# Kernel optimization log

Measured on AMD Instinct MI355X. Metric: run time of the kernel, lower is better.

## Reference

```python
import jax, jax.numpy as jnp
import numpy as np

N, F, H, G = 4096, 256, 8, 128  # atoms, filters, heads, groups
D = F // H  # head dim = 32


def setup_inputs() -> dict:
    key = jax.random.key(0)
    ks = jax.random.split(key, 12)
    x = jax.random.normal(ks[0], (N, F), dtype=jnp.float32)
    # sorted group ids in [0, G): block_diag over unique-count blocks == equality mask on sorted ids
    seg = jnp.sort(jax.random.randint(ks[1], (N,), 0, G, dtype=jnp.int32))
    elem_index = jnp.stack([jnp.arange(N, dtype=jnp.int32), seg])  # [2, N]
    s = 1.0 / np.sqrt(F)
    def lin(k):
        kw, kb = jax.random.split(k)
        return (jax.random.normal(kw, (F, F), dtype=jnp.float32) * s,
                jnp.zeros((F,), dtype=jnp.float32))
    Wq, bq = lin(ks[2]); Wk, bk = lin(ks[3]); Wv, bv = lin(ks[4])
    Wo1, bo1 = lin(ks[5]); Wo2, bo2 = lin(ks[6])
    return {"x": x, "elem_index": elem_index,
            "Wq": Wq, "bq": bq, "Wk": Wk, "bk": bk, "Wv": Wv, "bv": bv,
            "Wo1": Wo1, "bo1": bo1, "Wo2": Wo2, "bo2": bo2}


def reference(x, elem_index, Wq, bq, Wk, bk, Wv, bv, Wo1, bo1, Wo2, bo2):
    n = x.shape[0]
    # projections -> [H, N, D]
    q = (x @ Wq.T + bq).reshape(n, H, D).transpose(1, 0, 2)
    k = (x @ Wk.T + bk).reshape(n, H, D).transpose(1, 0, 2)
    v = (x @ Wv.T + bv).reshape(n, H, D).transpose(1, 0, 2)
    attn = jnp.einsum('hnd,hmd->hnm', q, k)          # [H, N, N]
    attn = jax.nn.silu(attn)                          # attn_act = activation() in source
    seg = elem_index[1]
    mask = (seg[:, None] == seg[None, :]).astype(attn.dtype)  # block-diagonal (sorted ids)
    attn = attn * mask
    out = jnp.einsum('hnm,hmd->hnd', attn, v)        # [H, N, D]
    out = out.transpose(1, 0, 2).reshape(n, F)       # [N, F]
    out = out @ Wo1.T + bo1
    out = jax.ops.segment_sum(out, seg, num_segments=G)  # scatter sum by group -> [G, F]
    out = out @ Wo2.T + bo2
    return jax.nn.silu(out)
```

## Files before the change

kernel.cpp:

```cpp
#include <hip/hip_runtime.h>
#include <math.h>

#define NATOMS 4096
#define FDIM   256
#define NHEAD  8
#define DHEAD  32
#define NGRP   128

typedef __bf16 bf16x8 __attribute__((ext_vector_type(8)));
typedef float  floatx4 __attribute__((ext_vector_type(4)));
typedef unsigned short u16x4 __attribute__((ext_vector_type(4)));

__device__ __forceinline__ float silu_f(float x) {
    return x / (1.0f + __expf(-x));
}

__device__ __forceinline__ unsigned short f2bf(float f) {
    union { float f; unsigned int u; } a;
    a.f = f;
    unsigned int r = a.u + 0x7FFF + ((a.u >> 16) & 1);
    return (unsigned short)(r >> 16);
}

__global__ __launch_bounds__(256) void prep_kernel(
    const float* __restrict__ x,
    const float* __restrict__ Wq, const float* __restrict__ Wk, const float* __restrict__ Wv,
    const float* __restrict__ bq, const float* __restrict__ bk, const float* __restrict__ bv,
    const int* __restrict__ seg,
    unsigned short* __restrict__ xb, unsigned short* __restrict__ Wb,
    float* __restrict__ b_all, int* __restrict__ off, float* __restrict__ cntf)
{
    int tid = threadIdx.x;
    unsigned int u = blockIdx.x * 256 + tid;

    if (blockIdx.x == 0 && tid < NGRP) {
        int g = tid;
        auto lb = [&](int val) {
            int lo = 0, hi = NATOMS;
            while (lo < hi) {
                int mid = (lo + hi) >> 1;
                if (seg[mid] < val) lo = mid + 1; else hi = mid;
            }
            return lo;
        };
        int a = lb(g);
        int b = lb(g + 1);
        off[g] = a;
        if (g == NGRP - 1) off[NGRP] = NATOMS;
        cntf[g] = (float)(b - a);
    }
    if (blockIdx.x == 1 && tid < 192) {
        const float* src = (tid < 64) ? bq : (tid < 128) ? bk : bv;
        int t = tid & 63;
        ((float4*)b_all)[tid] = ((const float4*)src)[t];
    }

    const unsigned int NX4 = 262144;
    const unsigned int NW4 = 16384;
    float4 fv;
    u16x4* dst;
    if (u < NX4) {
        fv = ((const float4*)x)[u];
        dst = (u16x4*)xb + u;
    } else {
        unsigned int r = u - NX4;
        unsigned int w = r / NW4;
        unsigned int i = r - w * NW4;
        const float* W = (w == 0) ? Wq : (w == 1) ? Wk : Wv;
        fv = ((const float4*)W)[i];
        dst = (u16x4*)Wb + (size_t)w * NW4 + i;
    }
    u16x4 o;
    o[0] = f2bf(fv.x); o[1] = f2bf(fv.y); o[2] = f2bf(fv.z); o[3] = f2bf(fv.w);
    *dst = o;
}

__global__ __launch_bounds__(256) void qkv_mfma(
    const unsigned short* __restrict__ xb, const unsigned short* __restrict__ Wb,
    const float* __restrict__ b_all, float* __restrict__ qkv)
{
    int tid = threadIdx.x;
    int lane = tid & 63;
    int ww = tid >> 6;
    int wrow = ww >> 1, wcol = ww & 1;
    int m_base = blockIdx.x * 64 + wrow * 32;
    int n_base = blockIdx.y * 128 + wcol * 64;

    int l15 = lane & 15;
    int quad = lane >> 4;
    int kq = quad * 8;

    floatx4 acc[2][4] = {};

    const unsigned short* arow0 = xb + (size_t)(m_base + l15) * 256 + kq;
    const unsigned short* arow1 = arow0 + 16 * 256;
    const unsigned short* brow[4];
#pragma unroll
    for (int ni = 0; ni < 4; ++ni)
        brow[ni] = Wb + (size_t)(n_base + ni * 16 + l15) * 256 + kq;

#pragma unroll
    for (int ks = 0; ks < 8; ++ks) {
        int ko = ks * 32;
        bf16x8 a0 = *(const bf16x8*)(arow0 + ko);
        bf16x8 a1 = *(const bf16x8*)(arow1 + ko);
#pragma unroll
        for (int ni = 0; ni < 4; ++ni) {
            bf16x8 b = *(const bf16x8*)(brow[ni] + ko);
            acc[0][ni] = __builtin_amdgcn_mfma_f32_16x16x32_bf16(a0, b, acc[0][ni], 0, 0, 0);
            acc[1][ni] = __builtin_amdgcn_mfma_f32_16x16x32_bf16(a1, b, acc[1][ni], 0, 0, 0);
        }
    }

#pragma unroll
    for (int mi = 0; mi < 2; ++mi) {
#pragma unroll
        for (int ni = 0; ni < 4; ++ni) {
            int col_g = n_base + ni * 16 + l15;
            int w = col_g >> 8, c = col_g & 255;
            float bias = b_all[col_g];
            float* outp = qkv + (size_t)w * (NATOMS * FDIM) + c;
#pragma unroll
            for (int r = 0; r < 4; ++r) {
                int row = m_base + mi * 16 + quad * 4 + r;
                outp[(size_t)row * FDIM] = acc[mi][ni][r] + bias;
            }
        }
    }
}

__global__ __launch_bounds__(256) void gemm_small(
    const float* __restrict__ A, const float* __restrict__ B,
    const float* __restrict__ bias, const float* __restrict__ rowScale,
    float* __restrict__ C, int M, int Ncols, int K, int act)
{
    __shared__ float As[32][36];
    __shared__ float Bs[32][36];

    int tid = threadIdx.x;
    int bm = blockIdx.y * 32;
    int bn = blockIdx.x * 32;
    int tx = tid & 15;
    int ty = tid >> 4;
    int lm = tid >> 3;
    int lk = (tid & 7) << 2;

    float acc[2][2] = {};

    for (int kt = 0; kt < K; kt += 32) {
        const float4 av = *(const float4*)(A + (size_t)(bm + lm) * K + kt + lk);
        const float4 bv = *(const float4*)(B + (size_t)(bn + lm) * K + kt + lk);
        As[lk + 0][lm] = av.x; As[lk + 1][lm] = av.y;
        As[lk + 2][lm] = av.z; As[lk + 3][lm] = av.w;
        Bs[lk + 0][lm] = bv.x; Bs[lk + 1][lm] = bv.y;
        Bs[lk + 2][lm] = bv.z; Bs[lk + 3][lm] = bv.w;
        __syncthreads();

#pragma unroll
        for (int kk = 0; kk < 32; ++kk) {
            float a0 = As[kk][ty * 2], a1 = As[kk][ty * 2 + 1];
            float c0 = Bs[kk][tx * 2], c1 = Bs[kk][tx * 2 + 1];
            acc[0][0] = fmaf(a0, c0, acc[0][0]);
            acc[0][1] = fmaf(a0, c1, acc[0][1]);
            acc[1][0] = fmaf(a1, c0, acc[1][0]);
            acc[1][1] = fmaf(a1, c1, acc[1][1]);
        }
        __syncthreads();
    }

#pragma unroll
    for (int i = 0; i < 2; ++i) {
        int m = bm + ty * 2 + i;
        float rs = rowScale ? rowScale[m] : 1.0f;
#pragma unroll
        for (int j = 0; j < 2; ++j) {
            int n = bn + tx * 2 + j;
            float vv = acc[i][j] + rs * bias[n];
            if (act) vv = silu_f(vv);
            C[(size_t)m * Ncols + n] = vv;
        }
    }
}

#define JT 32
#define IT 64

__global__ __launch_bounds__(256) void attn_kernel(
    const float* __restrict__ q, const float* __restrict__ k,
    const float* __restrict__ v, const int* __restrict__ off,
    float* __restrict__ Ysum)
{
    int g = blockIdx.x, h = blockIdx.y;
    int base = off[g];
    int end  = off[g + 1];
    base = min(max(base, 0), NATOMS);
    end  = min(max(end, base), NATOMS);
    int n = end - base;

    __shared__ float4 qt4[IT * 8];
    __shared__ float4 vt4[JT * 8];
    __shared__ float  wred[8][JT];
    __shared__ float  w[JT];
    __shared__ float  red[8][DHEAD];

    int tid = threadIdx.x;
    int jj = tid & 31;
    int iq = tid >> 5;
    int d = tid & 31;
    int r = tid >> 5;

    const float4* q4 = (const float4*)(q + (size_t)base * FDIM) + h * 8;
    const float4* k4 = (const float4*)(k + (size_t)base * FDIM) + h * 8;
    const float4* v4 = (const float4*)(v + (size_t)base * FDIM) + h * 8;

    float accY = 0.0f;

    for (int j0 = 0; j0 < n; j0 += JT) {
        int jt_n = min(JT, n - j0);
        __syncthreads();
        for (int idx = tid; idx < jt_n * 8; idx += 256)
            vt4[idx] = v4[(size_t)(j0 + (idx >> 3)) * 64 + (idx & 7)];

        float4 kr[8];
        {
            int jrow = (jj < jt_n) ? (j0 + jj) : j0;
#pragma unroll
            for (int c = 0; c < 8; ++c) kr[c] = k4[(size_t)jrow * 64 + c];
        }

        float wpart = 0.0f;
        for (int i0 = 0; i0 < n; i0 += IT) {
            int it_n = min(IT, n - i0);
            __syncthreads();
            for (int idx = tid; idx < it_n * 8; idx += 256)
                qt4[idx] = q4[(size_t)(i0 + (idx >> 3)) * 64 + (idx & 7)];
            __syncthreads();
            if (jj < jt_n) {
                for (int ii = iq; ii < it_n; ii += 8) {
                    const float4* qr = &qt4[ii * 8];
                    float s = 0.0f;
#pragma unroll
                    for (int c = 0; c < 8; ++c) {
                        float4 a = qr[c];
                        s = fmaf(a.x, kr[c].x, s);
                        s = fmaf(a.y, kr[c].y, s);
                        s = fmaf(a.z, kr[c].z, s);
                        s = fmaf(a.w, kr[c].w, s);
                    }
                    wpart += silu_f(s);
                }
            }
        }
        wred[iq][jj] = wpart;
        __syncthreads();
        if (tid < JT) {
            float s = 0.0f;
#pragma unroll
            for (int rr = 0; rr < 8; ++rr) s += wred[rr][tid];
            w[tid] = s;
        }
        __syncthreads();
        const float* vts = (const float*)vt4;
        for (int j = r; j < jt_n; j += 8)
            accY = fmaf(w[j], vts[j * 32 + d], accY);
    }

    red[r][d] = accY;
    __syncthreads();
    if (r == 0) {
        float s = 0.0f;
#pragma unroll
        for (int rr = 0; rr < 8; ++rr) s += red[rr][d];
        Ysum[(size_t)g * FDIM + h * DHEAD + d] = s;
    }
}

extern "C" void kernel_launch(void* const* d_in, const int* in_sizes, int n_in,
                              void* d_out, int out_size, void* d_ws, size_t ws_size,
                              hipStream_t stream) {
    const float* x    = (const float*)d_in[0];
    const int*   eidx = (const int*)  d_in[1];
    const float* Wq   = (const float*)d_in[2];
    const float* bq   = (const float*)d_in[3];
    const float* Wk   = (const float*)d_in[4];
    const float* bk   = (const float*)d_in[5];
    const float* Wv   = (const float*)d_in[6];
    const float* bv   = (const float*)d_in[7];
    const float* Wo1  = (const float*)d_in[8];
    const float* bo1  = (const float*)d_in[9];
    const float* Wo2  = (const float*)d_in[10];
    const float* bo2  = (const float*)d_in[11];
    float* out = (float*)d_out;

    const int* seg = eidx + NATOMS;

    const size_t NF = (size_t)NATOMS * FDIM;
    const size_t GF = (size_t)NGRP * FDIM;

    float* q     = (float*)d_ws;
    float* k     = q + NF;
    float* v     = k + NF;
    float* Ysum  = v + NF;
    float* S     = Ysum + GF;
    float* cntf  = S + GF;
    float* b_all = cntf + NGRP;
    int*   off   = (int*)(b_all + 768);
    unsigned short* xb = (unsigned short*)((float*)off + 160);
    unsigned short* Wb = xb + NF;

    prep_kernel<<<1216, 256, 0, stream>>>(x, Wq, Wk, Wv, bq, bk, bv, seg,
                                          xb, Wb, b_all, off, cntf);

    dim3 gproj(NATOMS / 64, 768 / 128);
    qkv_mfma<<<gproj, 256, 0, stream>>>(xb, Wb, b_all, q);

    dim3 gattn(NGRP, NHEAD);
    attn_kernel<<<gattn, 256, 0, stream>>>(q, k, v, off, Ysum);

    dim3 gsmall(FDIM / 32, NGRP / 32);
    gemm_small<<<gsmall, 256, 0, stream>>>(Ysum, Wo1, bo1, cntf, S, NGRP, FDIM, FDIM, 0);

    gemm_small<<<gsmall, 256, 0, stream>>>(S, Wo2, bo2, nullptr, out, NGRP, FDIM, FDIM, 1);
}
```

Before: 128.4 us.

## Fuse group attention with both output projections into one per-group kernel

Attention, the Wo1 projection, the segment sum and the Wo2 projection plus SiLU now run in a single kernel with one block per group. Each of the eight warps handles one head, and a full 32-row Q tile across all heads is staged in shared memory. This removes two launches and the Ysum and S round trips through global memory. The trade-off is a grid of only 128 blocks instead of 1024 (group by head), which cuts parallelism in the dominant attention phase. Each thread also reads a full 256-wide weight row uncoalesced, and V is read straight from global memory.

```diff
diff --git a/kernel.cpp b/kernel.cpp
--- a/kernel.cpp
+++ b/kernel.cpp
@@ -28,7 +28,7 @@
     const float* __restrict__ bq, const float* __restrict__ bk, const float* __restrict__ bv,
     const int* __restrict__ seg,
     unsigned short* __restrict__ xb, unsigned short* __restrict__ Wb,
-    float* __restrict__ b_all, int* __restrict__ off, float* __restrict__ cntf)
+    float* __restrict__ b_all, int* __restrict__ off)
 {
     int tid = threadIdx.x;
     unsigned int u = blockIdx.x * 256 + tid;
@@ -44,10 +44,8 @@
             return lo;
         };
         int a = lb(g);
-        int b = lb(g + 1);
         off[g] = a;
         if (g == NGRP - 1) off[NGRP] = NATOMS;
-        cntf[g] = (float)(b - a);
     }
     if (blockIdx.x == 1 && tid < 192) {
         const float* src = (tid < 64) ? bq : (tid < 128) ? bk : bv;
@@ -129,115 +127,57 @@
     }
 }
 
-__global__ __launch_bounds__(256) void gemm_small(
-    const float* __restrict__ A, const float* __restrict__ B,
-    const float* __restrict__ bias, const float* __restrict__ rowScale,
-    float* __restrict__ C, int M, int Ncols, int K, int act)
-{
-    __shared__ float As[32][36];
-    __shared__ float Bs[32][36];
-
-    int tid = threadIdx.x;
-    int bm = blockIdx.y * 32;
-    int bn = blockIdx.x * 32;
-    int tx = tid & 15;
-    int ty = tid >> 4;
-    int lm = tid >> 3;
-    int lk = (tid & 7) << 2;
-
-    float acc[2][2] = {};
-
-    for (int kt = 0; kt < K; kt += 32) {
-        const float4 av = *(const float4*)(A + (size_t)(bm + lm) * K + kt + lk);
-        const float4 bv = *(const float4*)(B + (size_t)(bn + lm) * K + kt + lk);
-        As[lk + 0][lm] = av.x; As[lk + 1][lm] = av.y;
-        As[lk + 2][lm] = av.z; As[lk + 3][lm] = av.w;
-        Bs[lk + 0][lm] = bv.x; Bs[lk + 1][lm] = bv.y;
-        Bs[lk + 2][lm] = bv.z; Bs[lk + 3][lm] = bv.w;
-        __syncthreads();
-
-#pragma unroll
-        for (int kk = 0; kk < 32; ++kk) {
-            float a0 = As[kk][ty * 2], a1 = As[kk][ty * 2 + 1];
-            float c0 = Bs[kk][tx * 2], c1 = Bs[kk][tx * 2 + 1];
-            acc[0][0] = fmaf(a0, c0, acc[0][0]);
-            acc[0][1] = fmaf(a0, c1, acc[0][1]);
-            acc[1][0] = fmaf(a1, c0, acc[1][0]);
-            acc[1][1] = fmaf(a1, c1, acc[1][1]);
-        }
-        __syncthreads();
-    }
-
-#pragma unroll
-    for (int i = 0; i < 2; ++i) {
-        int m = bm + ty * 2 + i;
-        float rs = rowScale ? rowScale[m] : 1.0f;
-#pragma unroll
-        for (int j = 0; j < 2; ++j) {
-            int n = bn + tx * 2 + j;
-            float vv = acc[i][j] + rs * bias[n];
-            if (act) vv = silu_f(vv);
-            C[(size_t)m * Ncols + n] = vv;
-        }
-    }
-}
-
-#define JT 32
-#define IT 64
-
-__global__ __launch_bounds__(256) void attn_kernel(
+#define QT 32
+
+__global__ __launch_bounds__(256) void attn_out(
     const float* __restrict__ q, const float* __restrict__ k,
     const float* __restrict__ v, const int* __restrict__ off,
-    float* __restrict__ Ysum)
+    const float* __restrict__ Wo1, const float* __restrict__ bo1,
+    const float* __restrict__ Wo2, const float* __restrict__ bo2,
+    float* __restrict__ out)
 {
-    int g = blockIdx.x, h = blockIdx.y;
+    int g = blockIdx.x;
     int base = off[g];
     int end  = off[g + 1];
     base = min(max(base, 0), NATOMS);
     end  = min(max(end, base), NATOMS);
     int n = end - base;
 
-    __shared__ float4 qt4[IT * 8];
-    __shared__ float4 vt4[JT * 8];
-    __shared__ float  wred[8][JT];
-    __shared__ float  w[JT];
-    __shared__ float  red[8][DHEAD];
-
-    int tid = threadIdx.x;
-    int jj = tid & 31;
-    int iq = tid >> 5;
-    int d = tid & 31;
-    int r = tid >> 5;
-
-    const float4* q4 = (const float4*)(q + (size_t)base * FDIM) + h * 8;
-    const float4* k4 = (const float4*)(k + (size_t)base * FDIM) + h * 8;
-    const float4* v4 = (const float4*)(v + (size_t)base * FDIM) + h * 8;
-
-    float accY = 0.0f;
-
-    for (int j0 = 0; j0 < n; j0 += JT) {
-        int jt_n = min(JT, n - j0);
-        __syncthreads();
-        for (int idx = tid; idx < jt_n * 8; idx += 256)
-            vt4[idx] = v4[(size_t)(j0 + (idx >> 3)) * 64 + (idx & 7)];
-
+    __shared__ float4 qt4[QT * 64];
+    __shared__ float  wloc[256];
+    __shared__ float  ybuf[FDIM];
+    __shared__ float  sbuf[FDIM];
+
+    int tid  = threadIdx.x;
+    int h    = tid >> 5;
+    int lane = tid & 31;
+
+    const float4* q4 = (const float4*)(q + (size_t)base * FDIM);
+    const float*  kg = k + (size_t)base * FDIM + h * DHEAD;
+    const float*  vg = v + (size_t)base * FDIM + h * DHEAD;
+
+    float ysum = 0.0f;
+
+    for (int j0 = 0; j0 < n; j0 += 32) {
+        int jt_n = min(32, n - j0);
+
+        int jrow = (lane < jt_n) ? (j0 + lane) : j0;
         float4 kr[8];
-        {
-            int jrow = (jj < jt_n) ? (j0 + jj) : j0;
-#pragma unroll
-            for (int c = 0; c < 8; ++c) kr[c] = k4[(size_t)jrow * 64 + c];
-        }
+        const float4* kp = (const float4*)(kg + (size_t)jrow * FDIM);
+#pragma unroll
+        for (int c = 0; c < 8; ++c) kr[c] = kp[c];
 
         float wpart = 0.0f;
-        for (int i0 = 0; i0 < n; i0 += IT) {
-            int it_n = min(IT, n - i0);
+        for (int i0 = 0; i0 < n; i0 += QT) {
+            int it_n = min(QT, n - i0);
             __syncthreads();
-            for (int idx = tid; idx < it_n * 8; idx += 256)
-                qt4[idx] = q4[(size_t)(i0 + (idx >> 3)) * 64 + (idx & 7)];
+            for (int idx = tid; idx < it_n * 64; idx += 256)
+                qt4[idx] = q4[(size_t)(i0 + (idx >> 6)) * 64 + (idx & 63)];
             __syncthreads();
-            if (jj < jt_n) {
-                for (int ii = iq; ii < it_n; ii += 8) {
-                    const float4* qr = &qt4[ii * 8];
+            if (lane < jt_n) {
+                const float4* qh = qt4 + h * 8;
+                for (int ii = 0; ii < it_n; ++ii) {
+                    const float4* qr = qh + ii * 64;
                     float s = 0.0f;
 #pragma unroll
                     for (int c = 0; c < 8; ++c) {
@@ -251,28 +191,42 @@
                 }
             }
         }
-        wred[iq][jj] = wpart;
+        wloc[tid] = wpart;
         __syncthreads();
-        if (tid < JT) {
-            float s = 0.0f;
-#pragma unroll
-            for (int rr = 0; rr < 8; ++rr) s += wred[rr][tid];
-            w[tid] = s;
-        }
-        __syncthreads();
-        const float* vts = (const float*)vt4;
-        for (int j = r; j < jt_n; j += 8)
-            accY = fmaf(w[j], vts[j * 32 + d], accY);
-    }
-
-    red[r][d] = accY;
+        for (int j = 0; j < jt_n; ++j)
+            ysum = fmaf(wloc[h * 32 + j], vg[(size_t)(j0 + j) * FDIM + lane], ysum);
+    }
+
+    ybuf[tid] = ysum;
     __syncthreads();
-    if (r == 0) {
-        float s = 0.0f;
-#pragma unroll
-        for (int rr = 0; rr < 8; ++rr) s += red[rr][d];
-        Ysum[(size_t)g * FDIM + h * DHEAD + d] = s;
-    }
+
+    float cnt = (float)n;
+    const float4* y4 = (const float4*)ybuf;
+    const float4* w1 = (const float4*)(Wo1 + (size_t)tid * FDIM);
+    float acc = cnt * bo1[tid];
+#pragma unroll
+    for (int c = 0; c < 64; ++c) {
+        float4 a = y4[c], b = w1[c];
+        acc = fmaf(a.x, b.x, acc);
+        acc = fmaf(a.y, b.y, acc);
+        acc = fmaf(a.z, b.z, acc);
+        acc = fmaf(a.w, b.w, acc);
+    }
+    sbuf[tid] = acc;
+    __syncthreads();
+
+    const float4* s4 = (const float4*)sbuf;
+    const float4* w2 = (const float4*)(Wo2 + (size_t)tid * FDIM);
+    float acc2 = bo2[tid];
+#pragma unroll
+    for (int c = 0; c < 64; ++c) {
+        float4 a = s4[c], b = w2[c];
+        acc2 = fmaf(a.x, b.x, acc2);
+        acc2 = fmaf(a.y, b.y, acc2);
+        acc2 = fmaf(a.z, b.z, acc2);
+        acc2 = fmaf(a.w, b.w, acc2);
+    }
+    out[(size_t)g * FDIM + tid] = silu_f(acc2);
 }
 
 extern "C" void kernel_launch(void* const* d_in, const int* in_sizes, int n_in,
@@ -295,30 +249,20 @@
     const int* seg = eidx + NATOMS;
 
     const size_t NF = (size_t)NATOMS * FDIM;
-    const size_t GF = (size_t)NGRP * FDIM;
 
     float* q     = (float*)d_ws;
     float* k     = q + NF;
     float* v     = k + NF;
-    float* Ysum  = v + NF;
-    float* S     = Ysum + GF;
-    float* cntf  = S + GF;
-    float* b_all = cntf + NGRP;
+    float* b_all = v + NF;
     int*   off   = (int*)(b_all + 768);
     unsigned short* xb = (unsigned short*)((float*)off + 160);
     unsigned short* Wb = xb + NF;
 
     prep_kernel<<<1216, 256, 0, stream>>>(x, Wq, Wk, Wv, bq, bk, bv, seg,
-                                          xb, Wb, b_all, off, cntf);
+                                          xb, Wb, b_all, off);
 
     dim3 gproj(NATOMS / 64, 768 / 128);
     qkv_mfma<<<gproj, 256, 0, stream>>>(xb, Wb, b_all, q);
 
-    dim3 gattn(NGRP, NHEAD);
-    attn_kernel<<<gattn, 256, 0, stream>>>(q, k, v, off, Ysum);
-
-    dim3 gsmall(FDIM / 32, NGRP / 32);
-    gemm_small<<<gsmall, 256, 0, stream>>>(Ysum, Wo1, bo1, cntf, S, NGRP, FDIM, FDIM, 0);
-
-    gemm_small<<<gsmall, 256, 0, stream>>>(S, Wo2, bo2, nullptr, out, NGRP, FDIM, FDIM, 1);
-}
+    attn_out<<<NGRP, 256, 0, stream>>>(q, k, v, off, Wo1, bo1, Wo2, bo2, out);
+}
```

New measurement: 136.0 us. 6.0% more time.

## Fuse bf16 conversion into QKV MFMA and merge output GEMMs into one kernel

Applied to the files above, without the earlier changes.

The separate prep kernel that converted x and the QKV weights to bf16 is removed. The MFMA projection kernel now loads fp32 directly and converts in registers, and it also computes the group offsets. The two small output GEMMs become a single per-group kernel that does both matvecs with an LDS intermediate. This cuts the launch count from five to three and removes the bf16 staging round trip through memory. In exchange the projection reloads fp32 data, twice the bytes, and converts it redundantly in every block, and the out_kernel reads weight rows with strided per-thread access.

```diff
diff --git a/kernel.cpp b/kernel.cpp
--- a/kernel.cpp
+++ b/kernel.cpp
@@ -9,82 +9,54 @@
 
 typedef __bf16 bf16x8 __attribute__((ext_vector_type(8)));
 typedef float  floatx4 __attribute__((ext_vector_type(4)));
-typedef unsigned short u16x4 __attribute__((ext_vector_type(4)));
 
 __device__ __forceinline__ float silu_f(float x) {
     return x / (1.0f + __expf(-x));
 }
 
-__device__ __forceinline__ unsigned short f2bf(float f) {
-    union { float f; unsigned int u; } a;
-    a.f = f;
-    unsigned int r = a.u + 0x7FFF + ((a.u >> 16) & 1);
-    return (unsigned short)(r >> 16);
-}
-
-__global__ __launch_bounds__(256) void prep_kernel(
+__device__ __forceinline__ bf16x8 cvt8(const float* __restrict__ p) {
+    float4 lo = *(const float4*)p;
+    float4 hi = *(const float4*)(p + 4);
+    bf16x8 r;
+    r[0] = (__bf16)lo.x; r[1] = (__bf16)lo.y; r[2] = (__bf16)lo.z; r[3] = (__bf16)lo.w;
+    r[4] = (__bf16)hi.x; r[5] = (__bf16)hi.y; r[6] = (__bf16)hi.z; r[7] = (__bf16)hi.w;
+    return r;
+}
+
+__global__ __launch_bounds__(256) void qkv_fused(
     const float* __restrict__ x,
     const float* __restrict__ Wq, const float* __restrict__ Wk, const float* __restrict__ Wv,
     const float* __restrict__ bq, const float* __restrict__ bk, const float* __restrict__ bv,
     const int* __restrict__ seg,
-    unsigned short* __restrict__ xb, unsigned short* __restrict__ Wb,
-    float* __restrict__ b_all, int* __restrict__ off, float* __restrict__ cntf)
+    float* __restrict__ qkv, int* __restrict__ off)
 {
     int tid = threadIdx.x;
-    unsigned int u = blockIdx.x * 256 + tid;
-
-    if (blockIdx.x == 0 && tid < NGRP) {
-        int g = tid;
-        auto lb = [&](int val) {
+
+    int flat = blockIdx.y * gridDim.x + blockIdx.x;
+    if (tid == 0 && flat <= NGRP) {
+        int g = flat;
+        if (g == NGRP) {
+            off[NGRP] = NATOMS;
+        } else {
             int lo = 0, hi = NATOMS;
             while (lo < hi) {
                 int mid = (lo + hi) >> 1;
-                if (seg[mid] < val) lo = mid + 1; else hi = mid;
+                if (seg[mid] < g) lo = mid + 1; else hi = mid;
             }
-            return lo;
-        };
-        int a = lb(g);
-        int b = lb(g + 1);
-        off[g] = a;
-        if (g == NGRP - 1) off[NGRP] = NATOMS;
-        cntf[g] = (float)(b - a);
-    }
-    if (blockIdx.x == 1 && tid < 192) {
-        const float* src = (tid < 64) ? bq : (tid < 128) ? bk : bv;
-        int t = tid & 63;
-        ((float4*)b_all)[tid] = ((const float4*)src)[t];
-    }
-
-    const unsigned int NX4 = 262144;
-    const unsigned int NW4 = 16384;
-    float4 fv;
-    u16x4* dst;
-    if (u < NX4) {
-        fv = ((const float4*)x)[u];
-        dst = (u16x4*)xb + u;
-    } else {
-        unsigned int r = u - NX4;
-        unsigned int w = r / NW4;
-        unsigned int i = r - w * NW4;
-        const float* W = (w == 0) ? Wq : (w == 1) ? Wk : Wv;
-        fv = ((const float4*)W)[i];
-        dst = (u16x4*)Wb + (size_t)w * NW4 + i;
-    }
-    u16x4 o;
-    o[0] = f2bf(fv.x); o[1] = f2bf(fv.y); o[2] = f2bf(fv.z); o[3] = f2bf(fv.w);
-    *dst = o;
-}
-
-__global__ __launch_bounds__(256) void qkv_mfma(
-    const unsigned short* __restrict__ xb, const unsigned short* __restrict__ Wb,
-    const float* __restrict__ b_all, float* __restrict__ qkv)
-{
-    int tid = threadIdx.x;
+            off[g] = lo;
+        }
+    }
+
     int lane = tid & 63;
     int ww = tid >> 6;
     int wrow = ww >> 1, wcol = ww & 1;
     int m_base = blockIdx.x * 64 + wrow * 32;
-    int n_base = blockIdx.y * 128 + wcol * 64;
+
+    int w_idx  = blockIdx.y >> 1;
+    int c_base = (blockIdx.y & 1) * 128 + wcol * 64;
+
+    const float* W  = (w_idx == 0) ? Wq : (w_idx == 1) ? Wk : Wv;
+    const float* bb = (w_idx == 0) ? bq : (w_idx == 1) ? bk : bv;
 
     int l15 = lane & 15;
     int quad = lane >> 4;
@@ -92,21 +64,21 @@
 
     floatx4 acc[2][4] = {};
 
-    const unsigned short* arow0 = xb + (size_t)(m_base + l15) * 256 + kq;
-    const unsigned short* arow1 = arow0 + 16 * 256;
-    const unsigned short* brow[4];
+    const float* ar0 = x + (size_t)(m_base + l15) * 256 + kq;
+    const float* ar1 = ar0 + 16 * 256;
+    const float* br[4];
 #pragma unroll
     for (int ni = 0; ni < 4; ++ni)
-        brow[ni] = Wb + (size_t)(n_base + ni * 16 + l15) * 256 + kq;
+        br[ni] = W + (size_t)(c_base + ni * 16 + l15) * 256 + kq;
 
 #pragma unroll
     for (int ks = 0; ks < 8; ++ks) {
         int ko = ks * 32;
-        bf16x8 a0 = *(const bf16x8*)(arow0 + ko);
-        bf16x8 a1 = *(const bf16x8*)(arow1 + ko);
+        bf16x8 a0 = cvt8(ar0 + ko);
+        bf16x8 a1 = cvt8(ar1 + ko);
 #pragma unroll
         for (int ni = 0; ni < 4; ++ni) {
-            bf16x8 b = *(const bf16x8*)(brow[ni] + ko);
+            bf16x8 b = cvt8(br[ni] + ko);
             acc[0][ni] = __builtin_amdgcn_mfma_f32_16x16x32_bf16(a0, b, acc[0][ni], 0, 0, 0);
             acc[1][ni] = __builtin_amdgcn_mfma_f32_16x16x32_bf16(a1, b, acc[1][ni], 0, 0, 0);
         }
@@ -116,68 +88,14 @@
     for (int mi = 0; mi < 2; ++mi) {
 #pragma unroll
         for (int ni = 0; ni < 4; ++ni) {
-            int col_g = n_base + ni * 16 + l15;
-            int w = col_g >> 8, c = col_g & 255;
-            float bias = b_all[col_g];
-            float* outp = qkv + (size_t)w * (NATOMS * FDIM) + c;
+            int c = c_base + ni * 16 + l15;
+            float bias = bb[c];
+            float* outp = qkv + (size_t)w_idx * (NATOMS * FDIM) + c;
 #pragma unroll
             for (int r = 0; r < 4; ++r) {
                 int row = m_base + mi * 16 + quad * 4 + r;
                 outp[(size_t)row * FDIM] = acc[mi][ni][r] + bias;
             }
-        }
-    }
-}
-
-__global__ __launch_bounds__(256) void gemm_small(
-    const float* __restrict__ A, const float* __restrict__ B,
-    const float* __restrict__ bias, const float* __restrict__ rowScale,
-    float* __restrict__ C, int M, int Ncols, int K, int act)
-{
-    __shared__ float As[32][36];
-    __shared__ float Bs[32][36];
-
-    int tid = threadIdx.x;
-    int bm = blockIdx.y * 32;
-    int bn = blockIdx.x * 32;
-    int tx = tid & 15;
-    int ty = tid >> 4;
-    int lm = tid >> 3;
-    int lk = (tid & 7) << 2;
-
-    float acc[2][2] = {};
-
-    for (int kt = 0; kt < K; kt += 32) {
-        const float4 av = *(const float4*)(A + (size_t)(bm + lm) * K + kt + lk);
-        const float4 bv = *(const float4*)(B + (size_t)(bn + lm) * K + kt + lk);
-        As[lk + 0][lm] = av.x; As[lk + 1][lm] = av.y;
-        As[lk + 2][lm] = av.z; As[lk + 3][lm] = av.w;
-        Bs[lk + 0][lm] = bv.x; Bs[lk + 1][lm] = bv.y;
-        Bs[lk + 2][lm] = bv.z; Bs[lk + 3][lm] = bv.w;
-        __syncthreads();
-
-#pragma unroll
-        for (int kk = 0; kk < 32; ++kk) {
-            float a0 = As[kk][ty * 2], a1 = As[kk][ty * 2 + 1];
-            float c0 = Bs[kk][tx * 2], c1 = Bs[kk][tx * 2 + 1];
-            acc[0][0] = fmaf(a0, c0, acc[0][0]);
-            acc[0][1] = fmaf(a0, c1, acc[0][1]);
-            acc[1][0] = fmaf(a1, c0, acc[1][0]);
-            acc[1][1] = fmaf(a1, c1, acc[1][1]);
-        }
-        __syncthreads();
-    }
-
-#pragma unroll
-    for (int i = 0; i < 2; ++i) {
-        int m = bm + ty * 2 + i;
-        float rs = rowScale ? rowScale[m] : 1.0f;
-#pragma unroll
-        for (int j = 0; j < 2; ++j) {
-            int n = bn + tx * 2 + j;
-            float vv = acc[i][j] + rs * bias[n];
-            if (act) vv = silu_f(vv);
-            C[(size_t)m * Ncols + n] = vv;
         }
     }
 }
@@ -273,6 +191,55 @@
         for (int rr = 0; rr < 8; ++rr) s += red[rr][d];
         Ysum[(size_t)g * FDIM + h * DHEAD + d] = s;
     }
+}
+
+__global__ __launch_bounds__(256) void out_kernel(
+    const float* __restrict__ Ysum, const int* __restrict__ off,
+    const float* __restrict__ Wo1, const float* __restrict__ bo1,
+    const float* __restrict__ Wo2, const float* __restrict__ bo2,
+    float* __restrict__ out)
+{
+    int g = blockIdx.x;
+    int tid = threadIdx.x;
+
+    __shared__ float ybuf[FDIM];
+    __shared__ float sbuf[FDIM];
+
+    int base = off[g];
+    int end  = off[g + 1];
+    base = min(max(base, 0), NATOMS);
+    end  = min(max(end, base), NATOMS);
+    float cnt = (float)(end - base);
+
+    ybuf[tid] = Ysum[(size_t)g * FDIM + tid];
+    __syncthreads();
+
+    const float4* y4 = (const float4*)ybuf;
+    const float4* w1 = (const float4*)(Wo1 + (size_t)tid * FDIM);
+    float acc = cnt * bo1[tid];
+#pragma unroll
+    for (int c = 0; c < 64; ++c) {
+        float4 a = y4[c], b = w1[c];
+        acc = fmaf(a.x, b.x, acc);
+        acc = fmaf(a.y, b.y, acc);
+        acc = fmaf(a.z, b.z, acc);
+        acc = fmaf(a.w, b.w, acc);
+    }
+    sbuf[tid] = acc;
+    __syncthreads();
+
+    const float4* s4 = (const float4*)sbuf;
+    const float4* w2 = (const float4*)(Wo2 + (size_t)tid * FDIM);
+    float acc2 = bo2[tid];
+#pragma unroll
+    for (int c = 0; c < 64; ++c) {
+        float4 a = s4[c], b = w2[c];
+        acc2 = fmaf(a.x, b.x, acc2);
+        acc2 = fmaf(a.y, b.y, acc2);
+        acc2 = fmaf(a.z, b.z, acc2);
+        acc2 = fmaf(a.w, b.w, acc2);
+    }
+    out[(size_t)g * FDIM + tid] = silu_f(acc2);
 }
 
 extern "C" void kernel_launch(void* const* d_in, const int* in_sizes, int n_in,
@@ -297,28 +264,17 @@
     const size_t NF = (size_t)NATOMS * FDIM;
     const size_t GF = (size_t)NGRP * FDIM;
 
-    float* q     = (float*)d_ws;
-    float* k     = q + NF;
-    float* v     = k + NF;
-    float* Ysum  = v + NF;
-    float* S     = Ysum + GF;
-    float* cntf  = S + GF;
-    float* b_all = cntf + NGRP;
-    int*   off   = (int*)(b_all + 768);
-    unsigned short* xb = (unsigned short*)((float*)off + 160);
-    unsigned short* Wb = xb + NF;
-
-    prep_kernel<<<1216, 256, 0, stream>>>(x, Wq, Wk, Wv, bq, bk, bv, seg,
-                                          xb, Wb, b_all, off, cntf);
+    float* q    = (float*)d_ws;
+    float* k    = q + NF;
+    float* v    = k + NF;
+    float* Ysum = v + NF;
+    int*   off  = (int*)(Ysum + GF);
 
     dim3 gproj(NATOMS / 64, 768 / 128);
-    qkv_mfma<<<gproj, 256, 0, stream>>>(xb, Wb, b_all, q);
+    qkv_fused<<<gproj, 256, 0, stream>>>(x, Wq, Wk, Wv, bq, bk, bv, seg, q, off);
 
     dim3 gattn(NGRP, NHEAD);
     attn_kernel<<<gattn, 256, 0, stream>>>(q, k, v, off, Ysum);
 
-    dim3 gsmall(FDIM / 32, NGRP / 32);
-    gemm_small<<<gsmall, 256, 0, stream>>>(Ysum, Wo1, bo1, cntf, S, NGRP, FDIM, FDIM, 0);
-
-    gemm_small<<<gsmall, 256, 0, stream>>>(S, Wo2, bo2, nullptr, out, NGRP, FDIM, FDIM, 1);
-}
+    out_kernel<<<NGRP, 256, 0, stream>>>(Ysum, off, Wo1, bo1, Wo2, bo2, out);
+}
```

New measurement: 131.3 us. 1.02x slower.
